# Performance work log

Hardware: AMD Instinct MI355X
Metric: run time of the kernel (lower is better)

## Reference

```python
import jax, jax.numpy as jnp
import numpy as np

B, T, C = 8, 1024, 2048
N_HEAD = 16
HEAD = C // N_HEAD  # 128


def setup_inputs() -> dict:
    key = jax.random.key(0)
    k1, k2, k3 = jax.random.split(key, 3)
    scale = 0.02
    x = jax.random.normal(k1, (B, T, C), dtype=jnp.float32)
    W_attn = jax.random.normal(k2, (C, 3 * C), dtype=jnp.float32) * scale
    b_attn = jnp.zeros((3 * C,), dtype=jnp.float32)
    W_proj = jax.random.normal(k3, (C, C), dtype=jnp.float32) * scale
    b_proj = jnp.zeros((C,), dtype=jnp.float32)
    return {"x": x, "W_attn": W_attn, "b_attn": b_attn, "W_proj": W_proj, "b_proj": b_proj}


def reference(x, W_attn, b_attn, W_proj, b_proj):
    Bq, Tq, Cq = x.shape
    qkv = x @ W_attn + b_attn                       # [B,T,3C]
    q, k, v = jnp.split(qkv, 3, axis=2)             # each [B,T,C]
    def heads(t):
        return t.reshape(Bq, Tq, N_HEAD, HEAD).transpose(0, 2, 1, 3)  # [B,H,T,D]
    q, k, v = heads(q), heads(k), heads(v)
    scores = jnp.einsum('bhqd,bhkd->bhqk', q, k) / jnp.sqrt(jnp.float32(HEAD))
    causal = jnp.tril(jnp.ones((Tq, Tq), dtype=bool))
    scores = jnp.where(causal, scores, jnp.float32(-1e9))
    attn = jax.nn.softmax(scores, axis=-1)          # [B,H,T,T]
    y = jnp.einsum('bhqk,bhkd->bhqd', attn, v)      # [B,H,T,D]
    y = y.transpose(0, 2, 1, 3).reshape(Bq, Tq, Cq) # [B,T,C]
    return y @ W_proj + b_proj
```

## Files before the change

### kernel.cpp

```cpp
#include <hip/hip_runtime.h>
#include <hip/hip_bf16.h>


typedef unsigned short u16;
typedef __bf16 bf16x8 __attribute__((ext_vector_type(8)));
typedef float f32x4 __attribute__((ext_vector_type(4)));

#define B_ 8
#define T_ 1024
#define C_ 2048
#define NH 16
#define HD 128
#define BH (B_*NH)

__device__ __forceinline__ u16 f2b(float f){
  __bf16 h = (__bf16)f; return __builtin_bit_cast(u16, h);
}
__device__ __forceinline__ unsigned pk2(float x, float y){
  return (unsigned)f2b(x) | ((unsigned)f2b(y) << 16);
}
__device__ __forceinline__ bf16x8 ldfrag(const u16* p){
  uint4 u = *(const uint4*)p; return __builtin_bit_cast(bf16x8, u);
}
__device__ __forceinline__ void glds16(const u16* g, const u16* l){
  __builtin_amdgcn_global_load_lds(
      (const __attribute__((address_space(1))) void*)g,
      (__attribute__((address_space(3))) void*)l, 16, 0, 0);
}

__global__ __launch_bounds__(256) void cvt_bf16(
    const float4* __restrict__ in, ushort4* __restrict__ outp, int n4)
{
  int i = blockIdx.x*256 + threadIdx.x;
  const int stride = gridDim.x*256;
  for (; i < n4; i += stride){
    float4 f = in[i];
    ushort4 o; o.x = f2b(f.x); o.y = f2b(f.y); o.z = f2b(f.z); o.w = f2b(f.w);
    outp[i] = o;
  }
}

__global__ __launch_bounds__(256) void transpose_cvt(
    const float* __restrict__ in, u16* __restrict__ outp, int R, int C)
{
  __shared__ u16 tile[64][65];
  const int t = threadIdx.x;
  const int r0 = blockIdx.y * 64, c0 = blockIdx.x * 64;
#pragma unroll
  for (int ii = 0; ii < 16; ++ii){
    int idx = t + ii*256; int r = idx >> 6, c = idx & 63;
    tile[r][c] = f2b(in[(size_t)(r0 + r)*C + c0 + c]);
  }
  __syncthreads();
#pragma unroll
  for (int ii = 0; ii < 16; ++ii){
    int idx = t + ii*256; int r = idx >> 6, c = idx & 63;
    outp[(size_t)(c0 + r)*R + r0 + c] = tile[c][r];
  }
}

__device__ __forceinline__ void qkv_epilogue(
    const f32x4 acc[4][4], const float* bias, int bx, int by,
    int wm, int wn, int lq, int ln,
    u16* qb, u16* kb, u16* vb)
{
  const int tensor = bx >> 4, h = bx & 15, b = by >> 3, t0 = (by & 7)*128;
  u16* tb = tensor==0 ? qb : (tensor==1 ? kb : vb);
  u16* op = tb + ((size_t)(b*NH + h)*T_ + t0)*HD;
#pragma unroll
  for (int j=0;j<4;j++){
    const float bv = bias[bx*128 + wn*64 + j*16 + ln];
    const int n = wn*64 + j*16 + ln;
#pragma unroll
    for (int i=0;i<4;i++){
      const int m0 = wm*64 + i*16 + lq*4;
#pragma unroll
      for (int r=0;r<4;r++)
        op[(size_t)(m0 + r)*HD + n] = f2b(acc[i][j][r] + bv);
    }
  }
}

__global__ __launch_bounds__(256,2) void gemm_qkv_bb(
    const u16* __restrict__ Xb, const u16* __restrict__ Wt, const float* __restrict__ bias,
    u16* __restrict__ qb, u16* __restrict__ kb, u16* __restrict__ vb)
{
  __shared__ u16 As[128*32];
  __shared__ u16 Bs[128*32];
  const int t = threadIdx.x;
  const int bx = blockIdx.x, by = blockIdx.y;
  const int lane = t & 63, wv = t >> 6;
  const int lq = lane >> 4, ln = lane & 15;
  const int wm = wv >> 1, wn = wv & 1;

  const int c0 = t, c1 = 256 + t;
  const u16* Ap0 = Xb + (size_t)(by*128 + (c0 >> 2))*2048 + (c0 & 3)*8;
  const u16* Ap1 = Xb + (size_t)(by*128 + (c1 >> 2))*2048 + (c1 & 3)*8;
  const u16* Bp0 = Wt + (size_t)(bx*128 + (c0 >> 2))*2048 + (c0 & 3)*8;
  const u16* Bp1 = Wt + (size_t)(bx*128 + (c1 >> 2))*2048 + (c1 & 3)*8;
  const u16* AsW0 = &As[(wv*64)*8];
  const u16* AsW1 = &As[(256 + wv*64)*8];
  const u16* BsW0 = &Bs[(wv*64)*8];
  const u16* BsW1 = &Bs[(256 + wv*64)*8];

  const f32x4 fz = {0.f,0.f,0.f,0.f};
  f32x4 acc[4][4];
#pragma unroll
  for (int i=0;i<4;i++)
#pragma unroll
    for (int j=0;j<4;j++) acc[i][j] = fz;

  for (int kt = 0; kt < 64; ++kt){
    __syncthreads();
    glds16(Ap0, AsW0); glds16(Ap1, AsW1);
    glds16(Bp0, BsW0); glds16(Bp1, BsW1);
    Ap0 += 32; Ap1 += 32; Bp0 += 32; Bp1 += 32;
    __syncthreads();
    bf16x8 af[4], bf[4];
#pragma unroll
    for (int i=0;i<4;i++) af[i] = ldfrag(&As[(wm*64 + i*16 + ln)*32 + lq*8]);
#pragma unroll
    for (int j=0;j<4;j++) bf[j] = ldfrag(&Bs[(wn*64 + j*16 + ln)*32 + lq*8]);
#pragma unroll
    for (int i=0;i<4;i++)
#pragma unroll
      for (int j=0;j<4;j++)
        acc[i][j] = __builtin_amdgcn_mfma_f32_16x16x32_bf16(af[i], bf[j], acc[i][j], 0,0,0);
  }
  qkv_epilogue(acc, bias, bx, by, wm, wn, lq, ln, qb, kb, vb);
}

__global__ __launch_bounds__(256,2) void gemm_qkv_f32(
    const float* __restrict__ X, const u16* __restrict__ Wt, const float* __restrict__ bias,
    u16* __restrict__ qb, u16* __restrict__ kb, u16* __restrict__ vb)
{
  __shared__ u16 As[128*32];
  __shared__ u16 Bs[128*32];
  const int t = threadIdx.x;
  const int bx = blockIdx.x, by = blockIdx.y;
  const int lane = t & 63, wv = t >> 6;
  const int lq = lane >> 4, ln = lane & 15;
  const int wm = wv >> 1, wn = wv & 1;

  const int ar = t >> 1, ah = t & 1;
  const float* Ap = X + (size_t)(by*128 + ar)*2048 + ah*16;
  u16* AsW = &As[ar*32 + ah*16];

  const int c0 = t, c1 = 256 + t;
  const u16* Bp0 = Wt + (size_t)(bx*128 + (c0 >> 2))*2048 + (c0 & 3)*8;
  const u16* Bp1 = Wt + (size_t)(bx*128 + (c1 >> 2))*2048 + (c1 & 3)*8;
  const u16* BsW0 = &Bs[(wv*64)*8];
  const u16* BsW1 = &Bs[(256 + wv*64)*8];

  const f32x4 fz = {0.f,0.f,0.f,0.f};
  f32x4 acc[4][4];
#pragma unroll
  for (int i=0;i<4;i++)
#pragma unroll
    for (int j=0;j<4;j++) acc[i][j] = fz;

  for (int kt = 0; kt < 64; ++kt){
    float4 a0 = *(const float4*)(Ap);
    float4 a1 = *(const float4*)(Ap + 4);
    float4 a2 = *(const float4*)(Ap + 8);
    float4 a3 = *(const float4*)(Ap + 12);
    Ap += 32;
    __syncthreads();
    uint4 w0, w1;
    w0.x = pk2(a0.x,a0.y); w0.y = pk2(a0.z,a0.w);
    w0.z = pk2(a1.x,a1.y); w0.w = pk2(a1.z,a1.w);
    w1.x = pk2(a2.x,a2.y); w1.y = pk2(a2.z,a2.w);
    w1.z = pk2(a3.x,a3.y); w1.w = pk2(a3.z,a3.w);
    *(uint4*)(AsW) = w0; *(uint4*)(AsW + 8) = w1;
    glds16(Bp0, BsW0);
    glds16(Bp1, BsW1);
    Bp0 += 32; Bp1 += 32;
    __syncthreads();
    bf16x8 af[4], bf[4];
#pragma unroll
    for (int i=0;i<4;i++) af[i] = ldfrag(&As[(wm*64 + i*16 + ln)*32 + lq*8]);
#pragma unroll
    for (int j=0;j<4;j++) bf[j] = ldfrag(&Bs[(wn*64 + j*16 + ln)*32 + lq*8]);
#pragma unroll
    for (int i=0;i<4;i++)
#pragma unroll
      for (int j=0;j<4;j++)
        acc[i][j] = __builtin_amdgcn_mfma_f32_16x16x32_bf16(af[i], bf[j], acc[i][j], 0,0,0);
  }
  qkv_epilogue(acc, bias, bx, by, wm, wn, lq, ln, qb, kb, vb);
}

__global__ __launch_bounds__(256,2) void gemm_proj(
    const u16* __restrict__ Y, const u16* __restrict__ Wt, const float* __restrict__ bias,
    float* __restrict__ outp)
{
  __shared__ u16 As[128*32];
  __shared__ u16 Bs[128*32];
  const int t = threadIdx.x;
  const int bx = blockIdx.x, by = blockIdx.y;
  const int lane = t & 63, wv = t >> 6;
  const int lq = lane >> 4, ln = lane & 15;
  const int wm = wv >> 1, wn = wv & 1;

  const int c0 = t, c1 = 256 + t;
  const int rA0 = by*128 + (c0 >> 2), rA1 = by*128 + (c1 >> 2);
  const u16* Ya0 = Y + ((size_t)((rA0 >> 10)*NH)*T_ + (rA0 & 1023))*HD;
  const u16* Ya1 = Y + ((size_t)((rA1 >> 10)*NH)*T_ + (rA1 & 1023))*HD;
  const int kc0 = (c0 & 3)*8, kc1 = (c1 & 3)*8;
  const u16* AsW0 = &As[(wv*64)*8];
  const u16* AsW1 = &As[(256 + wv*64)*8];

  const u16* Bp0 = Wt + (size_t)(bx*128 + (c0 >> 2))*2048 + (c0 & 3)*8;
  const u16* Bp1 = Wt + (size_t)(bx*128 + (c1 >> 2))*2048 + (c1 & 3)*8;
  const u16* BsW0 = &Bs[(wv*64)*8];
  const u16* BsW1 = &Bs[(256 + wv*64)*8];

  const f32x4 fz = {0.f,0.f,0.f,0.f};
  f32x4 acc[4][4];
#pragma unroll
  for (int i=0;i<4;i++)
#pragma unroll
    for (int j=0;j<4;j++) acc[i][j] = fz;

  for (int kt = 0; kt < 64; ++kt){
    __syncthreads();
    {
      const int k0 = kt*32 + kc0, k1 = kt*32 + kc1;
      glds16(Ya0 + (size_t)(k0 >> 7)*(T_*HD) + (k0 & 127), AsW0);
      glds16(Ya1 + (size_t)(k1 >> 7)*(T_*HD) + (k1 & 127), AsW1);
      glds16(Bp0, BsW0);
      glds16(Bp1, BsW1);
      Bp0 += 32; Bp1 += 32;
    }
    __syncthreads();
    bf16x8 af[4], bf[4];
#pragma unroll
    for (int i=0;i<4;i++) af[i] = ldfrag(&As[(wm*64 + i*16 + ln)*32 + lq*8]);
#pragma unroll
    for (int j=0;j<4;j++) bf[j] = ldfrag(&Bs[(wn*64 + j*16 + ln)*32 + lq*8]);
#pragma unroll
    for (int i=0;i<4;i++)
#pragma unroll
      for (int j=0;j<4;j++)
        acc[i][j] = __builtin_amdgcn_mfma_f32_16x16x32_bf16(af[i], bf[j], acc[i][j], 0,0,0);
  }

  float* op = outp + (size_t)(by*128)*2048 + bx*128;
#pragma unroll
  for (int j=0;j<4;j++){
    const float bv = bias[bx*128 + wn*64 + j*16 + ln];
    const int n = wn*64 + j*16 + ln;
#pragma unroll
    for (int i=0;i<4;i++){
      const int m0 = wm*64 + i*16 + lq*4;
#pragma unroll
      for (int r=0;r<4;r++)
        op[(size_t)(m0 + r)*2048 + n] = acc[i][j][r] + bv;
    }
  }
}

__global__ __launch_bounds__(256,2) void attn_fwd(
    u16* qy, const u16* __restrict__ kk, const u16* __restrict__ vv)
{
  __shared__ u16 Ks[64*128];
  __shared__ u16 Vt[128*64];
  __shared__ u16 Ps[4*32*64];
  const int qt = 7 - blockIdx.x, bh = blockIdx.y;
  const int t = threadIdx.x;
  const int lane = t & 63, wv = t >> 6;
  const int lq = lane >> 4, ln = lane & 15;

  bf16x8 qf[2][4];
#pragma unroll
  for (int i=0;i<2;i++)
#pragma unroll
    for (int kc=0;kc<4;kc++){
      int qrow = qt*128 + wv*32 + i*16 + ln;
      qf[i][kc] = ldfrag(&qy[((size_t)bh*T_ + qrow)*HD + kc*32 + lq*8]);
    }

  const f32x4 fz = {0.f,0.f,0.f,0.f};
  f32x4 o[2][8];
#pragma unroll
  for (int i=0;i<2;i++)
#pragma unroll
    for (int jd=0;jd<8;jd++) o[i][jd] = fz;
  float mi[2][4], li[2][4];
#pragma unroll
  for (int i=0;i<2;i++)
#pragma unroll
    for (int r=0;r<4;r++){ mi[i][r] = -1e30f; li[i][r] = 0.f; }

  const float scale = 0.08838834764831843f;
  const int kr = t & 63, dbase = (t >> 6)*32;
  const int nkt = 2*qt + 2;

  uint4 kreg[4];
  uint4 vreg[4];
  {
    const uint4* ksrc = (const uint4*)(kk + (size_t)bh*T_*HD);
#pragma unroll
    for (int ii=0; ii<4; ++ii) kreg[ii] = ksrc[t + ii*256];
#pragma unroll
    for (int ch=0; ch<4; ++ch)
      vreg[ch] = *(const uint4*)&vv[((size_t)bh*T_ + kr)*HD + dbase + ch*8];
  }

  for (int kt = 0; kt < nkt; ++kt){
    __syncthreads();
    uint4* kdst = (uint4*)Ks;
#pragma unroll
    for (int ii=0; ii<4; ++ii){
      const int c = t + ii*256;
      kdst[(c & ~15) | ((c & 15) ^ ((c >> 4) & 7))] = kreg[ii];
    }
#pragma unroll
    for (int ch=0; ch<4; ++ch){
      const u16* e = (const u16*)&vreg[ch];
#pragma unroll
      for (int j=0; j<8; ++j){
        const int d = dbase + ch*8 + j;
        Vt[d*64 + (kr ^ ((d & 7) << 3))] = e[j];
      }
    }
    __syncthreads();

    {
      const int ktn = (kt+1 < nkt) ? kt+1 : kt;
      const uint4* ksrc = (const uint4*)(kk + ((size_t)bh*T_ + ktn*64)*HD);
#pragma unroll
      for (int ii=0; ii<4; ++ii) kreg[ii] = ksrc[t + ii*256];
#pragma unroll
      for (int ch=0; ch<4; ++ch)
        vreg[ch] = *(const uint4*)&vv[((size_t)bh*T_ + ktn*64 + kr)*HD + dbase + ch*8];
    }

    f32x4 s[2][4];
#pragma unroll
    for (int i=0;i<2;i++)
#pragma unroll
      for (int j=0;j<4;j++) s[i][j] = fz;
    __builtin_amdgcn_s_setprio(1);
#pragma unroll
    for (int j=0;j<4;j++){
      bf16x8 kf[4];
      const int krow = j*16 + ln;
      const int ksw = (krow & 7) << 3;
#pragma unroll
      for (int kc=0;kc<4;kc++)
        kf[kc] = ldfrag(&Ks[krow*128 + ((kc*32 + lq*8) ^ ksw)]);
#pragma unroll
      for (int i=0;i<2;i++)
#pragma unroll
        for (int kc=0;kc<4;kc++)
          s[i][j] = __builtin_amdgcn_mfma_f32_16x16x32_bf16(qf[i][kc], kf[kc], s[i][j], 0,0,0);
    }
    __builtin_amdgcn_s_setprio(0);

#pragma unroll
    for (int i=0;i<2;i++)
#pragma unroll
      for (int j=0;j<4;j++)
#pragma unroll
        for (int r=0;r<4;r++){
          int qg = qt*128 + wv*32 + i*16 + lq*4 + r;
          int kg = kt*64 + j*16 + ln;
          float sv = s[i][j][r]*scale;
          s[i][j][r] = (kg > qg) ? -1e30f : sv;
        }

    float mxv[2][4];
#pragma unroll
    for (int i=0;i<2;i++)
#pragma unroll
      for (int r=0;r<4;r++){
        float mx = fmaxf(fmaxf(s[i][0][r], s[i][1][r]), fmaxf(s[i][2][r], s[i][3][r]));
        mx = fmaxf(mx, __shfl_xor(mx, 1));
        mx = fmaxf(mx, __shfl_xor(mx, 2));
        mx = fmaxf(mx, __shfl_xor(mx, 4));
        mx = fmaxf(mx, __shfl_xor(mx, 8));
        mxv[i][r] = mx;
      }
    bool ok = true;
#pragma unroll
    for (int i=0;i<2;i++)
#pragma unroll
      for (int r=0;r<4;r++) ok = ok && (mxv[i][r] <= mi[i][r] + 8.0f);
    if (!__all((int)ok)){
#pragma unroll
      for (int i=0;i<2;i++)
#pragma unroll
        for (int r=0;r<4;r++){
          float mnew = fmaxf(mi[i][r], mxv[i][r]);
          float alpha = __expf(mi[i][r] - mnew);
          li[i][r] *= alpha;
          mi[i][r] = mnew;
#pragma unroll
          for (int jd=0;jd<8;jd++) o[i][jd][r] *= alpha;
        }
    }
#pragma unroll
    for (int i=0;i<2;i++)
#pragma unroll
      for (int r=0;r<4;r++){
        float rs = 0.f;
#pragma unroll
        for (int j=0;j<4;j++){
          float p = __expf(s[i][j][r] - mi[i][r]);
          s[i][j][r] = p; rs += p;
        }
        rs += __shfl_xor(rs, 1); rs += __shfl_xor(rs, 2);
        rs += __shfl_xor(rs, 4); rs += __shfl_xor(rs, 8);
        li[i][r] += rs;
      }

#pragma unroll
    for (int i=0;i<2;i++)
#pragma unroll
      for (int j=0;j<4;j++)
#pragma unroll
        for (int r=0;r<4;r++){
          const int rr = i*16 + lq*4 + r;
          Ps[wv*2048 + rr*64 + ((j*16 + ln) ^ ((rr & 7) << 3))] = f2b(s[i][j][r]);
        }

    bf16x8 pf[2][2];
#pragma unroll
    for (int i=0;i<2;i++){
      const int prow = i*16 + ln;
      const int psw = (prow & 7) << 3;
#pragma unroll
      for (int kc=0;kc<2;kc++)
        pf[i][kc] = ldfrag(&Ps[wv*2048 + prow*64 + ((kc*32 + lq*8) ^ psw)]);
    }
    __builtin_amdgcn_s_setprio(1);
#pragma unroll
    for (int jd=0;jd<8;jd++){
      const int vrow = jd*16 + ln;
      const int vsw = (vrow & 7) << 3;
#pragma unroll
      for (int kc=0;kc<2;kc++){
        bf16x8 vf = ldfrag(&Vt[vrow*64 + ((kc*32 + lq*8) ^ vsw)]);
#pragma unroll
        for (int i=0;i<2;i++)
          o[i][jd] = __builtin_amdgcn_mfma_f32_16x16x32_bf16(pf[i][kc], vf, o[i][jd], 0,0,0);
      }
    }
    __builtin_amdgcn_s_setprio(0);
  }

#pragma unroll
  for (int i=0;i<2;i++)
#pragma unroll
    for (int r=0;r<4;r++){
      float inv = 1.f / li[i][r];
      int row = qt*128 + wv*32 + i*16 + lq*4 + r;
#pragma unroll
      for (int jd=0;jd<8;jd++)
        qy[((size_t)bh*T_ + row)*HD + jd*16 + ln] = f2b(o[i][jd][r] * inv);
    }
}

extern "C" void kernel_launch(void* const* d_in, const int* in_sizes, int n_in,
                              void* d_out, int out_size, void* d_ws, size_t ws_size,
                              hipStream_t stream)
{
  const float* x      = (const float*)d_in[0];
  const float* W_attn = (const float*)d_in[1];
  const float* b_attn = (const float*)d_in[2];
  const float* W_proj = (const float*)d_in[3];
  const float* b_proj = (const float*)d_in[4];
  float* out = (float*)d_out;

  u16* Wat = (u16*)d_ws;
  u16* Wpt = Wat + (size_t)6144*2048;
  u16* qb  = Wpt + (size_t)2048*2048;
  u16* xb  = qb  + (size_t)BH*T_*HD;
  u16* kb  = (u16*)d_out;
  u16* vb  = kb + (size_t)BH*T_*HD;

  const size_t need = ((size_t)6144*2048 + (size_t)2048*2048
                       + 2*(size_t)BH*T_*HD) * sizeof(u16);

  hipLaunchKernelGGL(transpose_cvt, dim3(96,32,1), dim3(256,1,1), 0, stream,
                     W_attn, Wat, 2048, 6144);
  hipLaunchKernelGGL(transpose_cvt, dim3(32,32,1), dim3(256,1,1), 0, stream,
                     W_proj, Wpt, 2048, 2048);
  if (ws_size >= need){
    hipLaunchKernelGGL(cvt_bf16, dim3(1024,1,1), dim3(256,1,1), 0, stream,
                       (const float4*)x, (ushort4*)xb, (B_*T_*C_)/4);
    hipLaunchKernelGGL(gemm_qkv_bb, dim3(48,64,1), dim3(256,1,1), 0, stream,
                       xb, Wat, b_attn, qb, kb, vb);
  } else {
    hipLaunchKernelGGL(gemm_qkv_f32, dim3(48,64,1), dim3(256,1,1), 0, stream,
                       x, Wat, b_attn, qb, kb, vb);
  }
  hipLaunchKernelGGL(attn_fwd, dim3(8,BH,1), dim3(256,1,1), 0, stream,
                     qb, kb, vb);
  hipLaunchKernelGGL(gemm_proj, dim3(16,64,1), dim3(256,1,1), 0, stream,
                     qb, Wpt, b_proj, out);
}
```

Before: 647.3 us.

## Rewrite QKV GEMM with 256x256 tiles, double-buffered LDS and 8-wave ping-pong schedule

Replaces the 128x128, single-buffered QKV GEMM with a 512-thread kernel computing 256x256 tiles over K steps of 64. It uses double-buffered LDS with XOR swizzling and staggers global-to-LDS loads between MFMA phases, using sched barriers, s_setprio and explicit vmcnt waits. It also remaps block IDs for L2 locality. The goal is to overlap memory with compute and raise data reuse, at the cost of 128KB of LDS per block and heavy register pressure from 32 accumulators per thread.

Result: faster. 627.8 us (-3.0%).

```diff
diff --git a/kernel.cpp b/kernel.cpp
--- a/kernel.cpp
+++ b/kernel.cpp
@@ -27,6 +27,11 @@
       (const __attribute__((address_space(1))) void*)g,
       (__attribute__((address_space(3))) void*)l, 16, 0, 0);
 }
+__device__ __forceinline__ void sbar(){
+  __builtin_amdgcn_sched_barrier(0);
+  __builtin_amdgcn_s_barrier();
+  __builtin_amdgcn_sched_barrier(0);
+}
 
 __global__ __launch_bounds__(256) void cvt_bf16(
     const float4* __restrict__ in, ushort4* __restrict__ outp, int n4)
@@ -81,53 +86,143 @@
   }
 }
 
-__global__ __launch_bounds__(256,2) void gemm_qkv_bb(
-    const u16* __restrict__ Xb, const u16* __restrict__ Wt, const float* __restrict__ bias,
+__global__ __launch_bounds__(512,2) void gemm_qkv_8p(
+    const u16* __restrict__ Xb, const u16* __restrict__ Wt,
+    const float* __restrict__ bias,
     u16* __restrict__ qb, u16* __restrict__ kb, u16* __restrict__ vb)
 {
-  __shared__ u16 As[128*32];
-  __shared__ u16 Bs[128*32];
+  __shared__ u16 lds[2][2][256*64];
   const int t = threadIdx.x;
-  const int bx = blockIdx.x, by = blockIdx.y;
-  const int lane = t & 63, wv = t >> 6;
+  const int lane = t & 63, wid = t >> 6;
   const int lq = lane >> 4, ln = lane & 15;
-  const int wm = wv >> 1, wn = wv & 1;
-
-  const int c0 = t, c1 = 256 + t;
-  const u16* Ap0 = Xb + (size_t)(by*128 + (c0 >> 2))*2048 + (c0 & 3)*8;
-  const u16* Ap1 = Xb + (size_t)(by*128 + (c1 >> 2))*2048 + (c1 & 3)*8;
-  const u16* Bp0 = Wt + (size_t)(bx*128 + (c0 >> 2))*2048 + (c0 & 3)*8;
-  const u16* Bp1 = Wt + (size_t)(bx*128 + (c1 >> 2))*2048 + (c1 & 3)*8;
-  const u16* AsW0 = &As[(wv*64)*8];
-  const u16* AsW1 = &As[(256 + wv*64)*8];
-  const u16* BsW0 = &Bs[(wv*64)*8];
-  const u16* BsW1 = &Bs[(256 + wv*64)*8];
+  const int wm = wid >> 2, wn = wid & 3;
+
+  const int bid0 = blockIdx.x;
+  const int bid = (bid0 & 7)*96 + (bid0 >> 3);
+  const int bx = bid % 24, by = bid / 24;
+
+  const int rl  = (wid << 4) + (lane >> 3);
+  const int sw0 = (lane & 7) ^ (rl & 7);
+  const int sw1 = (lane & 7) ^ ((rl + 8) & 7);
+  const u16* Ag = Xb + ((size_t)(by*256) + rl)*2048;
+  const u16* Bg = Wt + ((size_t)(bx*256) + rl)*2048;
+  const size_t q0off = (size_t)sw0*8;
+  const size_t q1off = (size_t)8*2048 + (size_t)sw1*8;
+
+#define STAGE(buf_, op_, h_, T_) do { \
+    const u16* s_ = (op_ ? Bg : Ag) + (size_t)(h_)*(128*2048) + (size_t)(T_)*64; \
+    const u16* d_ = &lds[buf_][op_][(((h_)*128) + (wid<<4))*64]; \
+    glds16(s_ + q0off, d_); \
+    glds16(s_ + q1off, d_ + 8*64); \
+  } while(0)
+
+  const int swr0 = (0*4 + lq) ^ (ln & 7);
+  const int swr1 = (1*4 + lq) ^ (ln & 7);
 
   const f32x4 fz = {0.f,0.f,0.f,0.f};
-  f32x4 acc[4][4];
-#pragma unroll
-  for (int i=0;i<4;i++)
-#pragma unroll
-    for (int j=0;j<4;j++) acc[i][j] = fz;
-
-  for (int kt = 0; kt < 64; ++kt){
-    __syncthreads();
-    glds16(Ap0, AsW0); glds16(Ap1, AsW1);
-    glds16(Bp0, BsW0); glds16(Bp1, BsW1);
-    Ap0 += 32; Ap1 += 32; Bp0 += 32; Bp1 += 32;
-    __syncthreads();
-    bf16x8 af[4], bf[4];
-#pragma unroll
-    for (int i=0;i<4;i++) af[i] = ldfrag(&As[(wm*64 + i*16 + ln)*32 + lq*8]);
-#pragma unroll
-    for (int j=0;j<4;j++) bf[j] = ldfrag(&Bs[(wn*64 + j*16 + ln)*32 + lq*8]);
-#pragma unroll
-    for (int i=0;i<4;i++)
-#pragma unroll
-      for (int j=0;j<4;j++)
-        acc[i][j] = __builtin_amdgcn_mfma_f32_16x16x32_bf16(af[i], bf[j], acc[i][j], 0,0,0);
-  }
-  qkv_epilogue(acc, bias, bx, by, wm, wn, lq, ln, qb, kb, vb);
+  f32x4 acc[8][4];
+#pragma unroll
+  for (int f=0;f<8;f++)
+#pragma unroll
+    for (int g=0;g<4;g++) acc[f][g] = fz;
+
+  STAGE(0,0,0,0); STAGE(0,0,1,0); STAGE(0,1,0,0); STAGE(0,1,1,0);
+  STAGE(1,1,0,1); STAGE(1,1,1,1); STAGE(1,0,0,1);
+  asm volatile("s_waitcnt vmcnt(6)" ::: "memory");
+  sbar();
+
+  for (int T = 0; T < 32; ++T){
+    const int b = T & 1;
+    const u16* As = lds[b][0];
+    const u16* Bs = lds[b][1];
+    bf16x8 a0[4][2], a4[4][2], bfr[4][2];
+
+#pragma unroll
+    for (int f=0;f<4;f++){
+      a0[f][0]  = ldfrag(&As[(wm*128 + f*16 + ln)*64 + swr0*8]);
+      a0[f][1]  = ldfrag(&As[(wm*128 + f*16 + ln)*64 + swr1*8]);
+      bfr[f][0] = ldfrag(&Bs[(wn*64  + f*16 + ln)*64 + swr0*8]);
+      bfr[f][1] = ldfrag(&Bs[(wn*64  + f*16 + ln)*64 + swr1*8]);
+    }
+    if (T+1 < 32) STAGE(b^1, 0, 1, T+1);
+    sbar();
+    __builtin_amdgcn_s_setprio(1);
+#pragma unroll
+    for (int f=0;f<4;f++)
+#pragma unroll
+      for (int g=0;g<2;g++){
+        acc[f][g] = __builtin_amdgcn_mfma_f32_16x16x32_bf16(a0[f][0], bfr[g][0], acc[f][g], 0,0,0);
+        acc[f][g] = __builtin_amdgcn_mfma_f32_16x16x32_bf16(a0[f][1], bfr[g][1], acc[f][g], 0,0,0);
+      }
+    __builtin_amdgcn_s_setprio(0);
+    sbar();
+
+#pragma unroll
+    for (int f=0;f<4;f++){
+      a4[f][0] = ldfrag(&As[(wm*128 + (f+4)*16 + ln)*64 + swr0*8]);
+      a4[f][1] = ldfrag(&As[(wm*128 + (f+4)*16 + ln)*64 + swr1*8]);
+    }
+    if (T+2 < 32) STAGE(b, 1, 0, T+2);
+    sbar();
+    __builtin_amdgcn_s_setprio(1);
+#pragma unroll
+    for (int f=0;f<4;f++)
+#pragma unroll
+      for (int g=0;g<2;g++){
+        acc[f+4][g] = __builtin_amdgcn_mfma_f32_16x16x32_bf16(a4[f][0], bfr[g][0], acc[f+4][g], 0,0,0);
+        acc[f+4][g] = __builtin_amdgcn_mfma_f32_16x16x32_bf16(a4[f][1], bfr[g][1], acc[f+4][g], 0,0,0);
+      }
+    __builtin_amdgcn_s_setprio(0);
+    sbar();
+
+    if (T+2 < 32) STAGE(b, 1, 1, T+2);
+    sbar();
+    __builtin_amdgcn_s_setprio(1);
+#pragma unroll
+    for (int f=0;f<4;f++)
+#pragma unroll
+      for (int g=2;g<4;g++){
+        acc[f+4][g] = __builtin_amdgcn_mfma_f32_16x16x32_bf16(a4[f][0], bfr[g][0], acc[f+4][g], 0,0,0);
+        acc[f+4][g] = __builtin_amdgcn_mfma_f32_16x16x32_bf16(a4[f][1], bfr[g][1], acc[f+4][g], 0,0,0);
+      }
+    __builtin_amdgcn_s_setprio(0);
+    sbar();
+
+    if (T+2 < 32) STAGE(b, 0, 0, T+2);
+    if (T >= 30) asm volatile("s_waitcnt vmcnt(0)" ::: "memory");
+    else         asm volatile("s_waitcnt vmcnt(6)" ::: "memory");
+    sbar();
+    __builtin_amdgcn_s_setprio(1);
+#pragma unroll
+    for (int f=0;f<4;f++)
+#pragma unroll
+      for (int g=2;g<4;g++){
+        acc[f][g] = __builtin_amdgcn_mfma_f32_16x16x32_bf16(a0[f][0], bfr[g][0], acc[f][g], 0,0,0);
+        acc[f][g] = __builtin_amdgcn_mfma_f32_16x16x32_bf16(a0[f][1], bfr[g][1], acc[f][g], 0,0,0);
+      }
+    __builtin_amdgcn_s_setprio(0);
+    sbar();
+  }
+#undef STAGE
+
+  const int tensor = bx >> 3;
+  u16* tb = tensor==0 ? qb : (tensor==1 ? kb : vb);
+  const int m_base = by*256 + wm*128;
+#pragma unroll
+  for (int g=0; g<4; ++g){
+    const int ncol = (bx & 7)*256 + wn*64 + g*16 + ln;
+    const float bv = bias[tensor*2048 + ncol];
+    const int h = ncol >> 7, d = ncol & 127;
+#pragma unroll
+    for (int f=0; f<8; ++f){
+      const int m0 = m_base + f*16 + lq*4;
+      const int bb = m0 >> 10, tt = m0 & 1023;
+      u16* op = tb + ((size_t)(bb*NH + h)*T_ + tt)*HD + d;
+#pragma unroll
+      for (int r=0;r<4;++r)
+        op[(size_t)r*HD] = f2b(acc[f][g][r] + bv);
+    }
+  }
 }
 
 __global__ __launch_bounds__(256,2) void gemm_qkv_f32(
@@ -490,7 +585,7 @@
   if (ws_size >= need){
     hipLaunchKernelGGL(cvt_bf16, dim3(1024,1,1), dim3(256,1,1), 0, stream,
                        (const float4*)x, (ushort4*)xb, (B_*T_*C_)/4);
-    hipLaunchKernelGGL(gemm_qkv_bb, dim3(48,64,1), dim3(256,1,1), 0, stream,
+    hipLaunchKernelGGL(gemm_qkv_8p, dim3(768,1,1), dim3(512,1,1), 0, stream,
                        xb, Wat, b_attn, qb, kb, vb);
   } else {
     hipLaunchKernelGGL(gemm_qkv_f32, dim3(48,64,1), dim3(256,1,1), 0, stream,
```
